# Performance work log

Hardware: AMD Instinct MI355X
Metric: run time of the kernel (lower is better)

## Reference

```python
import jax, jax.numpy as jnp
import numpy as np

# ---- geometry constants (from init_kwargs) ----
VOL_SHAPE = (96, 96, 96)        # (Z, Y, X)
VOL_SPACING = 1.0               # mm, isotropic
N_PROJ = 180
DET_ROWS, DET_COLS = 192, 384   # (v, u)
DET_SPACING_V, DET_SPACING_U = 1.0, 1.0
SID = 750.0                     # source-isocenter distance
SDD = 1200.0                    # source-detector distance


def _proj_matrices():
    """3x4 pinhole projection matrices for a circular cone-beam trajectory."""
    cu = (DET_COLS - 1) / 2.0
    cv = (DET_ROWS - 1) / 2.0
    Kc = np.array([[SDD / DET_SPACING_U, 0.0, cu],
                   [0.0, SDD / DET_SPACING_V, cv],
                   [0.0, 0.0, 1.0]])
    mats = []
    for th in np.linspace(0.0, 2.0 * np.pi, N_PROJ, endpoint=False):
        s = SID * np.array([np.cos(th), np.sin(th), 0.0])   # source position
        ez = -s / SID                                        # optical axis -> isocenter
        ex = np.array([-np.sin(th), np.cos(th), 0.0])        # detector u axis
        ey = np.array([0.0, 0.0, 1.0])                       # detector v axis
        R = np.stack([ex, ey, ez])                           # world -> camera
        P = Kc @ np.concatenate([R, (-R @ s)[:, None]], axis=1)
        mats.append(P)
    return np.stack(mats).astype(np.float32)                # [P, 3, 4]


def _voxel_coords():
    """Homogeneous world coordinates of all voxel centers, [4, N]."""
    zs = (np.arange(VOL_SHAPE[0]) - (VOL_SHAPE[0] - 1) / 2.0) * VOL_SPACING
    ys = (np.arange(VOL_SHAPE[1]) - (VOL_SHAPE[1] - 1) / 2.0) * VOL_SPACING
    xs = (np.arange(VOL_SHAPE[2]) - (VOL_SHAPE[2] - 1) / 2.0) * VOL_SPACING
    Z, Y, X = np.meshgrid(zs, ys, xs, indexing='ij')
    pts = np.stack([X.ravel(), Y.ravel(), Z.ravel(), np.ones(X.size)])
    return pts.astype(np.float32)


def _bilinear(img, u, v):
    """Zero-padded bilinear interpolation of img[H,W] at (v,u) pixel coords."""
    H, W = img.shape
    u0 = jnp.floor(u); v0 = jnp.floor(v)
    fu = u - u0; fv = v - v0
    u0i = u0.astype(jnp.int32); v0i = v0.astype(jnp.int32)
    def at(vi, ui):
        valid = (ui >= 0) & (ui < W) & (vi >= 0) & (vi < H)
        val = img[jnp.clip(vi, 0, H - 1), jnp.clip(ui, 0, W - 1)]
        return jnp.where(valid, val, jnp.zeros((), img.dtype))
    return (at(v0i, u0i) * (1 - fu) * (1 - fv)
            + at(v0i, u0i + 1) * fu * (1 - fv)
            + at(v0i + 1, u0i) * (1 - fu) * fv
            + at(v0i + 1, u0i + 1) * fu * fv)


def _backproject_one(sino, mats, coords):
    """sino [P,H,W], mats [P,3,4], coords [4,N] -> volume [Z,Y,X]."""
    N = coords.shape[1]
    @jax.checkpoint
    def step(acc, pm_s):
        P, s = pm_s
        uvw = P @ coords                      # [3, N]
        w = uvw[2]                            # ray depth along optical axis (>0)
        u = uvw[0] / w
        v = uvw[1] / w
        acc = acc + _bilinear(s, u, v) / (w * w)  # FDK distance weighting
        return acc, None
    acc, _ = jax.lax.scan(step, jnp.zeros((N,), sino.dtype), (mats, sino))
    return acc.reshape(VOL_SHAPE)


def setup_inputs() -> dict:
    key = jax.random.key(0)
    x = jax.random.normal(key, (2, N_PROJ, DET_ROWS, DET_COLS, 1), dtype=jnp.float32)
    proj_matrices = jnp.asarray(_proj_matrices())
    return {"x": x, "proj_matrices": proj_matrices}


def reference(x, proj_matrices):
    coords = jnp.asarray(_voxel_coords())                 # [4, N]
    sinos = jnp.squeeze(x, -1)                            # [B, P, H, W]
    vols = jax.vmap(lambda s: _backproject_one(s, proj_matrices, coords))(sinos)
    return vols[..., None]                                # [B, Z, Y, X, 1]
```

## Files before the change

### kernel.cpp

```cpp
#include <hip/hip_runtime.h>

#define NPROJ 180
#define DH 192
#define DW 384
#define VN 96
#define ZPER 4
#define TILE_U 64
#define TILE_V 14
#define TSIZE (TILE_U * TILE_V)
#define PSTRIDE (DH * DW)
#define BSTRIDE (NPROJ * DH * DW)

typedef float v2f __attribute__((ext_vector_type(2)));

__global__ __launch_bounds__(256) void cone_bp(
    const float* __restrict__ sino,
    const float* __restrict__ mats,
    float* __restrict__ out)
{
    __shared__ v2f tile2[2][2 * TSIZE];

    const int tid = threadIdx.x;
    const int x = blockIdx.x * 32 + ((tid & 7) | ((tid >> 6) << 3));
    const int y = blockIdx.y * 8 + ((tid >> 3) & 7);
    const int zc = blockIdx.z;

    const float xw = (float)x - 47.5f;
    const float yw = (float)y - 47.5f;
    const float zw0 = (float)(zc * ZPER) - 47.5f;

    const float xwc = (float)(blockIdx.x * 32) - 32.0f;
    const float ywc = (float)(blockIdx.y * 8) - 44.0f;
    const float zwc = (float)(zc * ZPER) - 46.0f;

    const float4* __restrict__ M = (const float4*)mats;

    int V[7];
#pragma unroll
    for (int k = 0; k < 7; ++k) {
        int li = tid + 256 * k;
        int bb = (li >= TSIZE) ? 1 : 0;
        int rem = li - bb * TSIZE;
        V[k] = bb * BSTRIDE + (rem >> 6) * DW + (rem & 63);
    }

#define ANCHOR(P, IU, IV)                                                   \
    {                                                                       \
        float4 a0 = M[(P) * 3 + 0];                                         \
        float4 a1 = M[(P) * 3 + 1];                                         \
        float4 a2 = M[(P) * 3 + 2];                                         \
        float unc = fmaf(a0.x, xwc, fmaf(a0.y, ywc, a0.w));                 \
        float vnc = fmaf(a1.x, xwc, fmaf(a1.y, ywc, fmaf(a1.z, zwc, a1.w)));\
        float wc  = fmaf(a2.x, xwc, fmaf(a2.y, ywc, a2.w));                 \
        float rwc = __builtin_amdgcn_rcpf(wc);                              \
        IU = __builtin_amdgcn_readfirstlane((int)floorf(unc * rwc) - 31);   \
        IV = __builtin_amdgcn_readfirstlane((int)floorf(vnc * rwc) - 6);    \
    }

    int siu, siv;
    ANCHOR(0, siu, siv)
    {
        const float* __restrict__ ps = sino + siv * DW + siu;
#pragma unroll
        for (int k = 0; k < 7; ++k)
            tile2[0][tid + 256 * k] = *(const v2f*)(ps + V[k]);
    }

    float acc0[ZPER], acc1[ZPER];
#pragma unroll
    for (int k = 0; k < ZPER; ++k) { acc0[k] = 0.0f; acc1[k] = 0.0f; }

    for (int p = 0; p < NPROJ; ++p) {
        __syncthreads();

        v2f g[7];
        int niu = siu, niv = siv;
        const bool has_next = (p + 1 < NPROJ);
        if (has_next) {
            ANCHOR(p + 1, niu, niv)
            const float* __restrict__ ps =
                sino + (p + 1) * PSTRIDE + niv * DW + niu;
#pragma unroll
            for (int k = 0; k < 7; ++k)
                g[k] = *(const v2f*)(ps + V[k]);
        }

        {
            float4 r0 = M[p * 3 + 0];
            float4 r1 = M[p * 3 + 1];
            float4 r2 = M[p * 3 + 2];
            float un  = fmaf(r0.x, xw, fmaf(r0.y, yw, r0.w));
            float vn0 = fmaf(r1.x, xw, fmaf(r1.y, yw, r1.w));
            float w   = fmaf(r2.x, xw, fmaf(r2.y, yw, r2.w));
            float rw  = __builtin_amdgcn_rcpf(w);
            float iw2 = rw * rw;
            float ul  = fmaf(un, rw, -(float)siu);
            float uf  = floorf(ul);
            float fu  = ul - uf;
            int   u0l = (int)uf;
            float vb  = fmaf(fmaf(r1.z, zw0, vn0), rw, -(float)siv);
            float dv  = r1.z * rw;

            const v2f* __restrict__ tb = tile2[p & 1];

            int   o[ZPER];
            float fv[ZPER];
#pragma unroll
            for (int k = 0; k < ZPER; ++k) {
                float v  = fmaf(dv, (float)k, vb);
                float vf = floorf(v);
                fv[k] = v - vf;
                o[k] = ((int)vf << 6) + u0l;
            }
            v2f A0[ZPER], B0[ZPER], A1[ZPER], B1[ZPER];
#pragma unroll
            for (int k = 0; k < ZPER; ++k) {
                A0[k] = tb[o[k]];
                B0[k] = tb[o[k] + TILE_U];
                A1[k] = tb[o[k] + TSIZE];
                B1[k] = tb[o[k] + TSIZE + TILE_U];
            }
#pragma unroll
            for (int k = 0; k < ZPER; ++k) {
                v2f C0 = A0[k] + (B0[k] - A0[k]) * fv[k];
                v2f C1 = A1[k] + (B1[k] - A1[k]) * fv[k];
                float h0 = fmaf(C0.y - C0.x, fu, C0.x);
                float h1 = fmaf(C1.y - C1.x, fu, C1.x);
                acc0[k] = fmaf(h0, iw2, acc0[k]);
                acc1[k] = fmaf(h1, iw2, acc1[k]);
            }
        }

        if (has_next) {
            v2f* __restrict__ dst = tile2[(p + 1) & 1];
#pragma unroll
            for (int k = 0; k < 7; ++k)
                dst[tid + 256 * k] = g[k];
        }
        siu = niu; siv = niv;
    }

    const int zbase = zc * ZPER;
#pragma unroll
    for (int k = 0; k < ZPER; ++k) {
        out[(((size_t)(zbase + k)) * VN + y) * VN + x] = acc0[k];
        out[(((size_t)(VN + zbase + k)) * VN + y) * VN + x] = acc1[k];
    }
#undef ANCHOR
}

extern "C" void kernel_launch(void* const* d_in, const int* in_sizes, int n_in,
                              void* d_out, int out_size, void* d_ws, size_t ws_size,
                              hipStream_t stream) {
    const float* sino = (const float*)d_in[0];
    const float* mats = (const float*)d_in[1];
    float* out = (float*)d_out;

    dim3 grid(VN / 32, VN / 8, VN / ZPER), block(256);
    hipLaunchKernelGGL(cone_bp, grid, block, 0, stream, sino, mats, out);
}
```

Baseline: 345.3 us.

## Split projections across two block halves with atomic accumulation and precomputed anchors

Doubles the grid by splitting the 180 projections into two halves, each block handling 90 and adding its partial sums to the output with float atomics after a memset. Tile anchors for all projections are precomputed once into shared memory instead of per iteration. Shared memory drops from a double buffer to a single buffer with two barriers per iteration, which removes the load/compute overlap across projections. The aim is more blocks for occupancy and latency hiding on a grid that was small (864 blocks), at the cost of a memset, atomics and an extra barrier per iteration.

Result: faster. 327.1 us (-5.3%).

```diff
diff --git a/kernel.cpp b/kernel.cpp
--- a/kernel.cpp
+++ b/kernel.cpp
@@ -1,6 +1,7 @@
 #include <hip/hip_runtime.h>
 
 #define NPROJ 180
+#define PHALF 90
 #define DH 192
 #define DW 384
 #define VN 96
@@ -8,6 +9,7 @@
 #define TILE_U 64
 #define TILE_V 14
 #define TSIZE (TILE_U * TILE_V)
+#define NPAIR (2 * TSIZE)
 #define PSTRIDE (DH * DW)
 #define BSTRIDE (NPROJ * DH * DW)
 
@@ -18,12 +20,15 @@
     const float* __restrict__ mats,
     float* __restrict__ out)
 {
-    __shared__ v2f tile2[2][2 * TSIZE];
+    __shared__ v2f tile2[NPAIR];
+    __shared__ int2 anch[PHALF];
 
     const int tid = threadIdx.x;
     const int x = blockIdx.x * 32 + ((tid & 7) | ((tid >> 6) << 3));
     const int y = blockIdx.y * 8 + ((tid >> 3) & 7);
-    const int zc = blockIdx.z;
+    const int half = (blockIdx.z >= 24) ? 1 : 0;
+    const int zc = blockIdx.z - 24 * half;
+    const int pbase = half * PHALF;
 
     const float xw = (float)x - 47.5f;
     const float yw = (float)y - 47.5f;
@@ -35,6 +40,19 @@
 
     const float4* __restrict__ M = (const float4*)mats;
 
+    if (tid < PHALF) {
+        int p = pbase + tid;
+        float4 a0 = M[p * 3 + 0];
+        float4 a1 = M[p * 3 + 1];
+        float4 a2 = M[p * 3 + 2];
+        float unc = fmaf(a0.x, xwc, fmaf(a0.y, ywc, a0.w));
+        float vnc = fmaf(a1.x, xwc, fmaf(a1.y, ywc, fmaf(a1.z, zwc, a1.w)));
+        float wc  = fmaf(a2.x, xwc, fmaf(a2.y, ywc, a2.w));
+        float rwc = __builtin_amdgcn_rcpf(wc);
+        anch[tid] = make_int2((int)floorf(unc * rwc) - 31,
+                              (int)floorf(vnc * rwc) - 6);
+    }
+
     int V[7];
 #pragma unroll
     for (int k = 0; k < 7; ++k) {
@@ -44,48 +62,48 @@
         V[k] = bb * BSTRIDE + (rem >> 6) * DW + (rem & 63);
     }
 
-#define ANCHOR(P, IU, IV)                                                   \
-    {                                                                       \
-        float4 a0 = M[(P) * 3 + 0];                                         \
-        float4 a1 = M[(P) * 3 + 1];                                         \
-        float4 a2 = M[(P) * 3 + 2];                                         \
-        float unc = fmaf(a0.x, xwc, fmaf(a0.y, ywc, a0.w));                 \
-        float vnc = fmaf(a1.x, xwc, fmaf(a1.y, ywc, fmaf(a1.z, zwc, a1.w)));\
-        float wc  = fmaf(a2.x, xwc, fmaf(a2.y, ywc, a2.w));                 \
-        float rwc = __builtin_amdgcn_rcpf(wc);                              \
-        IU = __builtin_amdgcn_readfirstlane((int)floorf(unc * rwc) - 31);   \
-        IV = __builtin_amdgcn_readfirstlane((int)floorf(vnc * rwc) - 6);    \
+    __syncthreads();
+
+    int cu, cv;
+    {
+        int2 a = anch[0];
+        cu = __builtin_amdgcn_readfirstlane(a.x);
+        cv = __builtin_amdgcn_readfirstlane(a.y);
     }
-
-    int siu, siv;
-    ANCHOR(0, siu, siv)
+    v2f g[7];
     {
-        const float* __restrict__ ps = sino + siv * DW + siu;
+        const float* __restrict__ ps = sino + pbase * PSTRIDE + cv * DW + cu;
 #pragma unroll
         for (int k = 0; k < 7; ++k)
-            tile2[0][tid + 256 * k] = *(const v2f*)(ps + V[k]);
+            g[k] = *(const v2f*)(ps + V[k]);
     }
 
     float acc0[ZPER], acc1[ZPER];
 #pragma unroll
     for (int k = 0; k < ZPER; ++k) { acc0[k] = 0.0f; acc1[k] = 0.0f; }
 
-    for (int p = 0; p < NPROJ; ++p) {
+    for (int i = 0; i < PHALF; ++i) {
+        __syncthreads();
+#pragma unroll
+        for (int k = 0; k < 7; ++k)
+            tile2[tid + 256 * k] = g[k];
+        const float nfu = -(float)cu;
+        const float nfv = -(float)cv;
         __syncthreads();
 
-        v2f g[7];
-        int niu = siu, niv = siv;
-        const bool has_next = (p + 1 < NPROJ);
-        if (has_next) {
-            ANCHOR(p + 1, niu, niv)
+        if (i + 1 < PHALF) {
+            int2 a = anch[i + 1];
+            cu = __builtin_amdgcn_readfirstlane(a.x);
+            cv = __builtin_amdgcn_readfirstlane(a.y);
             const float* __restrict__ ps =
-                sino + (p + 1) * PSTRIDE + niv * DW + niu;
+                sino + (pbase + i + 1) * PSTRIDE + cv * DW + cu;
 #pragma unroll
             for (int k = 0; k < 7; ++k)
                 g[k] = *(const v2f*)(ps + V[k]);
         }
 
         {
+            const int p = pbase + i;
             float4 r0 = M[p * 3 + 0];
             float4 r1 = M[p * 3 + 1];
             float4 r2 = M[p * 3 + 2];
@@ -94,14 +112,12 @@
             float w   = fmaf(r2.x, xw, fmaf(r2.y, yw, r2.w));
             float rw  = __builtin_amdgcn_rcpf(w);
             float iw2 = rw * rw;
-            float ul  = fmaf(un, rw, -(float)siu);
+            float ul  = fmaf(un, rw, nfu);
             float uf  = floorf(ul);
             float fu  = ul - uf;
             int   u0l = (int)uf;
-            float vb  = fmaf(fmaf(r1.z, zw0, vn0), rw, -(float)siv);
+            float vb  = fmaf(fmaf(r1.z, zw0, vn0), rw, nfv);
             float dv  = r1.z * rw;
-
-            const v2f* __restrict__ tb = tile2[p & 1];
 
             int   o[ZPER];
             float fv[ZPER];
@@ -115,10 +131,10 @@
             v2f A0[ZPER], B0[ZPER], A1[ZPER], B1[ZPER];
 #pragma unroll
             for (int k = 0; k < ZPER; ++k) {
-                A0[k] = tb[o[k]];
-                B0[k] = tb[o[k] + TILE_U];
-                A1[k] = tb[o[k] + TSIZE];
-                B1[k] = tb[o[k] + TSIZE + TILE_U];
+                A0[k] = tile2[o[k]];
+                B0[k] = tile2[o[k] + TILE_U];
+                A1[k] = tile2[o[k] + TSIZE];
+                B1[k] = tile2[o[k] + TSIZE + TILE_U];
             }
 #pragma unroll
             for (int k = 0; k < ZPER; ++k) {
@@ -130,23 +146,16 @@
                 acc1[k] = fmaf(h1, iw2, acc1[k]);
             }
         }
-
-        if (has_next) {
-            v2f* __restrict__ dst = tile2[(p + 1) & 1];
-#pragma unroll
-            for (int k = 0; k < 7; ++k)
-                dst[tid + 256 * k] = g[k];
-        }
-        siu = niu; siv = niv;
     }
 
     const int zbase = zc * ZPER;
 #pragma unroll
     for (int k = 0; k < ZPER; ++k) {
-        out[(((size_t)(zbase + k)) * VN + y) * VN + x] = acc0[k];
-        out[(((size_t)(VN + zbase + k)) * VN + y) * VN + x] = acc1[k];
+        unsafeAtomicAdd(&out[(((size_t)(zbase + k)) * VN + y) * VN + x],
+                        acc0[k]);
+        unsafeAtomicAdd(&out[(((size_t)(VN + zbase + k)) * VN + y) * VN + x],
+                        acc1[k]);
     }
-#undef ANCHOR
 }
 
 extern "C" void kernel_launch(void* const* d_in, const int* in_sizes, int n_in,
@@ -156,6 +165,8 @@
     const float* mats = (const float*)d_in[1];
     float* out = (float*)d_out;
 
-    dim3 grid(VN / 32, VN / 8, VN / ZPER), block(256);
+    hipMemsetAsync(out, 0, (size_t)out_size * sizeof(float), stream);
+
+    dim3 grid(VN / 32, VN / 8, 48), block(256);
     hipLaunchKernelGGL(cone_bp, grid, block, 0, stream, sino, mats, out);
 }
```
